# Kernel optimization log

Measured on AMD Instinct MI355X. Metric: run time of the kernel, lower is better.

The kernel has to match this reference:

```python
import jax, jax.numpy as jnp
import numpy as np

DIM = 1024
NUM_HEADS = 16
HEAD_DIM = DIM // NUM_HEADS
SCALE = HEAD_DIM ** (-0.5)


def alibi_slopes(num_heads):
    x = (2 ** 8) ** (1.0 / num_heads)
    return jnp.array([1.0 / x ** (i + 1) for i in range(num_heads)], dtype=jnp.float32)


def setup_inputs() -> dict:
    key = jax.random.key(0)
    ks = jax.random.split(key, 6)
    B, N = 2, 2048
    x = jax.random.normal(ks[0], (B, N, DIM), dtype=jnp.float32)
    s = DIM ** -0.5
    Wq = jax.random.normal(ks[1], (DIM, DIM), dtype=jnp.float32) * s
    Wk = jax.random.normal(ks[2], (DIM, DIM), dtype=jnp.float32) * s
    Wv = jax.random.normal(ks[3], (DIM, DIM), dtype=jnp.float32) * s
    Wp = jax.random.normal(ks[4], (DIM, DIM), dtype=jnp.float32) * s
    bp = jnp.zeros((DIM,), dtype=jnp.float32)
    return {"x": x, "Wq": Wq, "Wk": Wk, "Wv": Wv, "Wp": Wp, "bp": bp}


def reference(x, Wq, Wk, Wv, Wp, bp):
    B, N, C = x.shape
    H, D = NUM_HEADS, HEAD_DIM
    # Linear layers use torch convention: y = x @ W.T
    q = (x @ Wq.T).reshape(B, N, H, D).transpose(0, 2, 1, 3)  # [B,H,N,D]
    k = (x @ Wk.T).reshape(B, N, H, D).transpose(0, 2, 1, 3)
    v = (x @ Wv.T).reshape(B, N, H, D).transpose(0, 2, 1, 3)
    # ALiBi bias: slopes[h] * (j - i), shape [H,N,N]
    rel = (jnp.arange(N)[None, :] - jnp.arange(N)[:, None]).astype(jnp.float32)
    bias = alibi_slopes(H)[:, None, None] * rel  # [H,N,N]
    # NOTE: original code DIVIDES by scale (= head_dim**-0.5), i.e. multiplies by sqrt(D)
    score = jnp.einsum("bhnd,bhmd->bhnm", q, k) / SCALE + bias[None]
    attn = jax.nn.softmax(score, axis=-1)
    out = jnp.einsum("bhnm,bhmd->bhnd", attn, v)
    out = out.transpose(0, 2, 1, 3).reshape(B, N, C)
    return out @ Wp.T + bp
```

## Files before the change

### kernel.cpp

```cpp
#include <hip/hip_runtime.h>
#include <hip/hip_bf16.h>
#include <cstdint>
#include <cstddef>

#define BB 2
#define NN 2048
#define CC 1024
#define HH 16
#define DD 64
#define MM (BB*NN)

typedef __attribute__((ext_vector_type(8))) _Float16 half8;
typedef __attribute__((ext_vector_type(4))) _Float16 half4;
typedef __attribute__((ext_vector_type(4))) float f32x4;

__device__ __forceinline__ float exp2_fast(float x) {
    float r; asm("v_exp_f32 %0, %1" : "=v"(r) : "v"(x)); return r;
}

__device__ __forceinline__ void gl_lds16(const void* g, void* l) {
    __builtin_amdgcn_global_load_lds(
        (const __attribute__((address_space(1))) unsigned int*)g,
        (__attribute__((address_space(3))) unsigned int*)l, 16, 0, 0);
}

__global__ __launch_bounds__(256) void cvtAll(
    const float* __restrict__ x, const float* __restrict__ wq,
    const float* __restrict__ wk, const float* __restrict__ wv,
    const float* __restrict__ wp, _Float16* __restrict__ X16,
    _Float16* __restrict__ W16) {
    const int NX4 = MM * CC / 4;
    const int NW4 = CC * CC / 4;
    int i = blockIdx.x * 256 + threadIdx.x;
    const float4* src;
    half4* dst;
    if (i < NX4) {
        src = (const float4*)x + i;
        dst = (half4*)X16 + i;
    } else {
        int j = i - NX4;
        int s = j >> 18, off = j & (NW4 - 1);
        const float* wsel = (s == 0) ? wq : (s == 1) ? wk : (s == 2) ? wv : wp;
        src = (const float4*)wsel + off;
        dst = (half4*)(W16 + (size_t)s * CC * CC) + off;
    }
    float4 v = *src;
    half4 h = { (_Float16)v.x, (_Float16)v.y, (_Float16)v.z, (_Float16)v.w };
    *dst = h;
}

__global__ __launch_bounds__(256) void gemmQKV(
    const _Float16* __restrict__ A, const _Float16* __restrict__ B,
    _Float16* __restrict__ QH, _Float16* __restrict__ KH,
    _Float16* __restrict__ VT, float qscale) {
    __shared__ _Float16 sA[128 * 64];
    __shared__ _Float16 sB[128 * 64];
    const int K = CC;

    const int t = threadIdx.x;
    const int id = blockIdx.y * gridDim.x + blockIdx.x;
    const int xcd = id & 7, kk = id >> 3;
    const int bm = xcd * 4 + (kk & 3);
    const int bn = kk >> 2;
    const int w = t >> 6, lane = t & 63;
    const int wr = (w >> 1) * 64, wc = (w & 1) * 64;
    const int lr = lane & 15, lg = lane >> 4;

    f32x4 acc[4][4];
#pragma unroll
    for (int a = 0; a < 4; ++a)
#pragma unroll
        for (int b2 = 0; b2 < 4; ++b2)
#pragma unroll
            for (int e = 0; e < 4; ++e) acc[a][b2][e] = 0.f;

    for (int kt = 0; kt < K; kt += 64) {
#pragma unroll
        for (int p = 0; p < 4; ++p) {
            int u = p * 256 + t;
            int rowu = u >> 3, su = (u & 7) ^ (rowu & 7);
            gl_lds16(A + (size_t)(bm * 128 + rowu) * K + kt + su * 8, sA + u * 8);
            gl_lds16(B + (size_t)(bn * 128 + rowu) * K + kt + su * 8, sB + u * 8);
        }
        __syncthreads();

#pragma unroll
        for (int c = 0; c < 2; ++c) {
            half8 af[4], bf[4];
#pragma unroll
            for (int f = 0; f < 4; ++f) {
                int ra = wr + f * 16 + lr;
                af[f] = *(const half8*)((const char*)sA + ((ra * 128 + c * 64 + lg * 16) ^ ((ra & 7) << 4)));
                int rb = wc + f * 16 + lr;
                bf[f] = *(const half8*)((const char*)sB + ((rb * 128 + c * 64 + lg * 16) ^ ((rb & 7) << 4)));
            }
#pragma unroll
            for (int fi = 0; fi < 4; ++fi)
#pragma unroll
                for (int fj = 0; fj < 4; ++fj)
                    acc[fi][fj] = __builtin_amdgcn_mfma_f32_16x16x32_f16(af[fi], bf[fj], acc[fi][fj], 0, 0, 0);
        }
        __syncthreads();
    }

#pragma unroll
    for (int fi = 0; fi < 4; ++fi)
#pragma unroll
        for (int fj = 0; fj < 4; ++fj) {
            int col = bn * 128 + wc + fj * 16 + lr;
            int sel = col >> 10, c10 = col & 1023;
            int h2 = c10 >> 6, d2 = c10 & 63;
            int rowb = bm * 128 + wr + fi * 16 + lg * 4;
            int b2 = rowb >> 11, n2 = rowb & (NN - 1);
            if (sel == 0) {
#pragma unroll
                for (int e = 0; e < 4; ++e)
                    QH[((size_t)(b2 * HH + h2) * NN + n2 + e) * DD + d2] =
                        (_Float16)(acc[fi][fj][e] * qscale);
            } else if (sel == 1) {
#pragma unroll
                for (int e = 0; e < 4; ++e)
                    KH[((size_t)(b2 * HH + h2) * NN + n2 + e) * DD + d2] =
                        (_Float16)acc[fi][fj][e];
            } else {
                half4 pk = { (_Float16)acc[fi][fj][0], (_Float16)acc[fi][fj][1],
                             (_Float16)acc[fi][fj][2], (_Float16)acc[fi][fj][3] };
                *(half4*)(VT + ((size_t)(b2 * HH + h2) * DD + d2) * NN + n2) = pk;
            }
        }
}

__global__ __launch_bounds__(256) void gemmPROJ(
    const _Float16* __restrict__ A, const _Float16* __restrict__ B,
    const float* __restrict__ bias, float* __restrict__ Cout) {
    __shared__ _Float16 sA[128 * 64];
    __shared__ _Float16 sB[64 * 64];
    const int K = CC, N = CC;

    const int t = threadIdx.x;
    const int id = blockIdx.y * gridDim.x + blockIdx.x;
    const int xcd = id & 7, kk = id >> 3;
    const int bm = xcd * 4 + (kk & 3);
    const int bn = kk >> 2;
    const int w = t >> 6, lane = t & 63;
    const int wr = (w >> 1) * 64, wc = (w & 1) * 32;
    const int lr = lane & 15, lg = lane >> 4;

    f32x4 acc[4][2];
#pragma unroll
    for (int a = 0; a < 4; ++a)
#pragma unroll
        for (int b2 = 0; b2 < 2; ++b2)
#pragma unroll
            for (int e = 0; e < 4; ++e) acc[a][b2][e] = 0.f;

    for (int kt = 0; kt < K; kt += 64) {
#pragma unroll
        for (int p = 0; p < 4; ++p) {
            int u = p * 256 + t;
            int rowu = u >> 3, su = (u & 7) ^ (rowu & 7);
            gl_lds16(A + (size_t)(bm * 128 + rowu) * K + kt + su * 8, sA + u * 8);
        }
#pragma unroll
        for (int p = 0; p < 2; ++p) {
            int u = p * 256 + t;
            int rowu = u >> 3, su = (u & 7) ^ (rowu & 7);
            gl_lds16(B + (size_t)(bn * 64 + rowu) * K + kt + su * 8, sB + u * 8);
        }
        __syncthreads();

#pragma unroll
        for (int c = 0; c < 2; ++c) {
            half8 af[4], bf[2];
#pragma unroll
            for (int f = 0; f < 4; ++f) {
                int ra = wr + f * 16 + lr;
                af[f] = *(const half8*)((const char*)sA + ((ra * 128 + c * 64 + lg * 16) ^ ((ra & 7) << 4)));
            }
#pragma unroll
            for (int f = 0; f < 2; ++f) {
                int rb = wc + f * 16 + lr;
                bf[f] = *(const half8*)((const char*)sB + ((rb * 128 + c * 64 + lg * 16) ^ ((rb & 7) << 4)));
            }
#pragma unroll
            for (int fi = 0; fi < 4; ++fi)
#pragma unroll
                for (int fj = 0; fj < 2; ++fj)
                    acc[fi][fj] = __builtin_amdgcn_mfma_f32_16x16x32_f16(af[fi], bf[fj], acc[fi][fj], 0, 0, 0);
        }
        __syncthreads();
    }

#pragma unroll
    for (int fi = 0; fi < 4; ++fi)
#pragma unroll
        for (int fj = 0; fj < 2; ++fj)
#pragma unroll
            for (int e = 0; e < 4; ++e) {
                int row = bm * 128 + wr + fi * 16 + lg * 4 + e;
                int col = bn * 64 + wc + fj * 16 + lr;
                Cout[(size_t)row * N + col] = acc[fi][fj][e] + bias[col];
            }
}

__global__ __launch_bounds__(256, 8) void attn16(
    const _Float16* __restrict__ Qh, const _Float16* __restrict__ Kh,
    const _Float16* __restrict__ Vt, _Float16* __restrict__ AO) {
    __shared__ _Float16 sK[2][64 * 64];
    __shared__ _Float16 sV[2][64 * 64];
    __shared__ _Float16 sP[4][16 * 64];

    const int t = threadIdx.x, w = t >> 6, lane = t & 63;
    const int lr = lane & 15, lg = lane >> 4;
    const int bh = blockIdx.x, qb = blockIdx.y;
    const int b = bh >> 4, h = bh & 15;
    const int i0 = qb * 64;
    const size_t baseND = (size_t)bh * NN * DD;
    const size_t baseDN = (size_t)bh * DD * NN;

    half8 qf[2];
    {
        const size_t qoff = baseND + (size_t)(i0 + w * 16 + lr) * DD;
        qf[0] = *(const half8*)(Qh + qoff + 0 * 32 + lg * 8);
        qf[1] = *(const half8*)(Qh + qoff + 1 * 32 + lg * 8);
    }

    f32x4 accO[4];
#pragma unroll
    for (int e = 0; e < 4; ++e)
        accO[e][0] = accO[e][1] = accO[e][2] = accO[e][3] = 0.f;
    float m_run = -INFINITY, l_run = 0.f;

    const float slope2 = exp2f(-0.5f * (float)(h + 1)) * 1.44269504f;
    const float s64 = slope2 * 64.f;
    f32x4 cini[4];
#pragma unroll
    for (int ct = 0; ct < 4; ++ct)
#pragma unroll
        for (int e = 0; e < 4; ++e)
            cini[ct][e] = slope2 * (float)(ct * 16 + lg * 4 + e);

    auto stage = [&](int buf, int jt) {
#pragma unroll
        for (int p = 0; p < 2; ++p) {
            int u = p * 256 + t;
            int rowu = u >> 3, su = (u & 7) ^ (rowu & 7);
            gl_lds16(Kh + baseND + (size_t)(jt * 64 + rowu) * DD + su * 8, &sK[buf][u * 8]);
            gl_lds16(Vt + baseDN + (size_t)rowu * NN + jt * 64 + su * 8, &sV[buf][u * 8]);
        }
    };

    stage(0, 0);
    __syncthreads();
    int cur = 0;
    float tb = 0.f;

    for (int jt = 0; jt < NN / 64; ++jt) {
        if (jt + 1 < NN / 64) stage(cur ^ 1, jt + 1);

        f32x4 s[4];
#pragma unroll
        for (int ct = 0; ct < 4; ++ct)
#pragma unroll
            for (int e = 0; e < 4; ++e) s[ct][e] = tb + cini[ct][e];

        __builtin_amdgcn_s_setprio(1);
#pragma unroll
        for (int ct = 0; ct < 4; ++ct)
#pragma unroll
            for (int c = 0; c < 2; ++c) {
                int row = ct * 16 + lr;
                half8 kf = *(const half8*)((const char*)&sK[cur][0] +
                    ((row * 128 + c * 64 + lg * 16) ^ ((row & 7) << 4)));
                s[ct] = __builtin_amdgcn_mfma_f32_16x16x32_f16(kf, qf[c], s[ct], 0, 0, 0);
            }
        __builtin_amdgcn_s_setprio(0);

        float x0 = fmaxf(fmaxf(s[0][0], s[0][1]), fmaxf(s[0][2], s[0][3]));
        float x1 = fmaxf(fmaxf(s[1][0], s[1][1]), fmaxf(s[1][2], s[1][3]));
        float x2 = fmaxf(fmaxf(s[2][0], s[2][1]), fmaxf(s[2][2], s[2][3]));
        float x3 = fmaxf(fmaxf(s[3][0], s[3][1]), fmaxf(s[3][2], s[3][3]));
        float mx = fmaxf(fmaxf(x0, x1), fmaxf(x2, x3));
        mx = fmaxf(mx, __shfl_xor(mx, 16, 64));
        mx = fmaxf(mx, __shfl_xor(mx, 32, 64));
        float mnew = fmaxf(m_run, mx);
        float al = exp2_fast(m_run - mnew);
#pragma unroll
        for (int ct = 0; ct < 4; ++ct)
#pragma unroll
            for (int e = 0; e < 4; ++e) s[ct][e] = exp2_fast(s[ct][e] - mnew);
        float y0 = (s[0][0] + s[0][1]) + (s[0][2] + s[0][3]);
        float y1 = (s[1][0] + s[1][1]) + (s[1][2] + s[1][3]);
        float y2 = (s[2][0] + s[2][1]) + (s[2][2] + s[2][3]);
        float y3 = (s[3][0] + s[3][1]) + (s[3][2] + s[3][3]);
        float sum = (y0 + y1) + (y2 + y3);
        sum += __shfl_xor(sum, 16, 64);
        sum += __shfl_xor(sum, 32, 64);
        m_run = mnew;
        l_run = l_run * al + sum;

#pragma unroll
        for (int ct = 0; ct < 4; ++ct) {
            unsigned plo = __builtin_bit_cast(unsigned,
                __builtin_amdgcn_cvt_pkrtz(s[ct][0], s[ct][1]));
            unsigned phi = __builtin_bit_cast(unsigned,
                __builtin_amdgcn_cvt_pkrtz(s[ct][2], s[ct][3]));
            uint2 pk = { plo, phi };
            *(uint2*)((char*)sP[w] + ((lr * 128 + ct * 32 + lg * 8) ^ ((lr & 7) << 4))) = pk;
        }

#pragma unroll
        for (int ctd = 0; ctd < 4; ++ctd)
#pragma unroll
            for (int e = 0; e < 4; ++e) accO[ctd][e] *= al;

        half8 pb0 = *(const half8*)((const char*)sP[w] + ((lr * 128 + 0 * 64 + lg * 16) ^ ((lr & 7) << 4)));
        half8 pb1 = *(const half8*)((const char*)sP[w] + ((lr * 128 + 1 * 64 + lg * 16) ^ ((lr & 7) << 4)));
        __builtin_amdgcn_s_setprio(1);
#pragma unroll
        for (int ctd = 0; ctd < 4; ++ctd)
#pragma unroll
            for (int c = 0; c < 2; ++c) {
                int row = ctd * 16 + lr;
                half8 vf = *(const half8*)((const char*)&sV[cur][0] +
                    ((row * 128 + c * 64 + lg * 16) ^ ((row & 7) << 4)));
                accO[ctd] = __builtin_amdgcn_mfma_f32_16x16x32_f16(vf, c ? pb1 : pb0, accO[ctd], 0, 0, 0);
            }
        __builtin_amdgcn_s_setprio(0);

        __syncthreads();
        cur ^= 1;
        tb += s64;
    }

    float rl = 1.0f / l_run;
    const size_t obase = ((size_t)b * NN + i0 + w * 16 + lr) * CC + h * DD;
#pragma unroll
    for (int ctd = 0; ctd < 4; ++ctd) {
        half4 ov = { (_Float16)(accO[ctd][0] * rl), (_Float16)(accO[ctd][1] * rl),
                     (_Float16)(accO[ctd][2] * rl), (_Float16)(accO[ctd][3] * rl) };
        *(half4*)(AO + obase + ctd * 16 + lg * 4) = ov;
    }
}

extern "C" void kernel_launch(void* const* d_in, const int* in_sizes, int n_in,
                              void* d_out, int out_size, void* d_ws, size_t ws_size,
                              hipStream_t stream) {
    const float* x  = (const float*)d_in[0];
    const float* Wq = (const float*)d_in[1];
    const float* Wk = (const float*)d_in[2];
    const float* Wv = (const float*)d_in[3];
    const float* Wp = (const float*)d_in[4];
    const float* bp = (const float*)d_in[5];
    float* out = (float*)d_out;

    char* ws = (char*)d_ws;
    const size_t MB = 1024 * 1024;
    _Float16* X16 = (_Float16*)(ws + 0 * MB);
    _Float16* W16 = (_Float16*)(ws + 8 * MB);
    _Float16* QH  = (_Float16*)(ws + 16 * MB);
    _Float16* KH  = (_Float16*)(ws + 24 * MB);
    _Float16* VT  = (_Float16*)(ws + 32 * MB);
    _Float16* AO  = (_Float16*)(ws + 40 * MB);
    _Float16* WP16 = W16 + 3 * 1024 * 1024;

    cvtAll<<<8192, 256, 0, stream>>>(x, Wq, Wk, Wv, Wp, X16, W16);

    const float QSCALE = 8.0f * 1.44269504f;
    gemmQKV<<<dim3(3 * CC / 128, MM / 128), 256, 0, stream>>>(X16, W16, QH, KH, VT, QSCALE);

    attn16<<<dim3(BB * HH, NN / 64), 256, 0, stream>>>(QH, KH, VT, AO);

    gemmPROJ<<<dim3(CC / 64, MM / 128), 256, 0, stream>>>(AO, WP16, bp, out);
}
```

Before: 143.6 us.

## Split attention into producer and consumer warps with pipelined QK and PV

Rewrites the attention kernel as warp-specialized: four producer waves compute QK^T scores and the softmax for 32 query rows each, while four consumer waves do the PV MFMAs one tile behind. Probabilities and rescale factors pass through double-buffered LDS. Each block now covers 128 queries with 512 threads, which halves K/V reloads per query. The cost is more LDS, fewer blocks, and a possible imbalance between producer and consumer work.

```diff
diff --git a/kernel.cpp b/kernel.cpp
--- a/kernel.cpp
+++ b/kernel.cpp
@@ -203,143 +203,181 @@
             }
 }
 
-__global__ __launch_bounds__(256, 8) void attn16(
+__global__ __launch_bounds__(512, 4) void attnPC(
     const _Float16* __restrict__ Qh, const _Float16* __restrict__ Kh,
     const _Float16* __restrict__ Vt, _Float16* __restrict__ AO) {
     __shared__ _Float16 sK[2][64 * 64];
     __shared__ _Float16 sV[2][64 * 64];
-    __shared__ _Float16 sP[4][16 * 64];
+    __shared__ _Float16 sP[2][4][32 * 64];
+    __shared__ float sAl[2][4][32];
+    __shared__ float sL[4][32];
 
     const int t = threadIdx.x, w = t >> 6, lane = t & 63;
     const int lr = lane & 15, lg = lane >> 4;
     const int bh = blockIdx.x, qb = blockIdx.y;
     const int b = bh >> 4, h = bh & 15;
-    const int i0 = qb * 64;
+    const int i0 = qb * 128;
     const size_t baseND = (size_t)bh * NN * DD;
     const size_t baseDN = (size_t)bh * DD * NN;
-
-    half8 qf[2];
-    {
-        const size_t qoff = baseND + (size_t)(i0 + w * 16 + lr) * DD;
-        qf[0] = *(const half8*)(Qh + qoff + 0 * 32 + lg * 8);
-        qf[1] = *(const half8*)(Qh + qoff + 1 * 32 + lg * 8);
-    }
-
-    f32x4 accO[4];
-#pragma unroll
-    for (int e = 0; e < 4; ++e)
-        accO[e][0] = accO[e][1] = accO[e][2] = accO[e][3] = 0.f;
-    float m_run = -INFINITY, l_run = 0.f;
+    const bool isProd = (w < 4);
+    const int pw = w & 3;
 
     const float slope2 = exp2f(-0.5f * (float)(h + 1)) * 1.44269504f;
-    const float s64 = slope2 * 64.f;
-    f32x4 cini[4];
-#pragma unroll
-    for (int ct = 0; ct < 4; ++ct)
-#pragma unroll
-        for (int e = 0; e < 4; ++e)
-            cini[ct][e] = slope2 * (float)(ct * 16 + lg * 4 + e);
-
-    auto stage = [&](int buf, int jt) {
-#pragma unroll
-        for (int p = 0; p < 2; ++p) {
-            int u = p * 256 + t;
-            int rowu = u >> 3, su = (u & 7) ^ (rowu & 7);
-            gl_lds16(Kh + baseND + (size_t)(jt * 64 + rowu) * DD + su * 8, &sK[buf][u * 8]);
-            gl_lds16(Vt + baseDN + (size_t)rowu * NN + jt * 64 + su * 8, &sV[buf][u * 8]);
-        }
+    const float s64v = slope2 * 64.f;
+    const float s16v = slope2 * 16.f;
+    float cini0[4];
+#pragma unroll
+    for (int e = 0; e < 4; ++e) cini0[e] = slope2 * (float)(lg * 4 + e);
+
+    auto stageK = [&](int buf, int jt) {
+        int rowu = t >> 3, su = (t & 7) ^ (rowu & 7);
+        gl_lds16(Kh + baseND + (size_t)(jt * 64 + rowu) * DD + su * 8, &sK[buf][t * 8]);
     };
-
-    stage(0, 0);
-    __syncthreads();
-    int cur = 0;
-    float tb = 0.f;
-
-    for (int jt = 0; jt < NN / 64; ++jt) {
-        if (jt + 1 < NN / 64) stage(cur ^ 1, jt + 1);
-
-        f32x4 s[4];
-#pragma unroll
-        for (int ct = 0; ct < 4; ++ct)
-#pragma unroll
-            for (int e = 0; e < 4; ++e) s[ct][e] = tb + cini[ct][e];
-
+    auto stageV = [&](int buf, int jt) {
+        int rowu = t >> 3, su = (t & 7) ^ (rowu & 7);
+        gl_lds16(Vt + baseDN + (size_t)rowu * NN + jt * 64 + su * 8, &sV[buf][t * 8]);
+    };
+
+    half8 qf[2][2];
+    float m_run[2], l_run[2], tbp = 0.f;
+    f32x4 accO[2][4];
+
+    if (isProd) {
+#pragma unroll
+        for (int u = 0; u < 2; ++u) {
+            const size_t qoff = baseND + (size_t)(i0 + pw * 32 + u * 16 + lr) * DD;
+            qf[u][0] = *(const half8*)(Qh + qoff + 0 * 32 + lg * 8);
+            qf[u][1] = *(const half8*)(Qh + qoff + 1 * 32 + lg * 8);
+        }
+        m_run[0] = m_run[1] = -INFINITY;
+        l_run[0] = l_run[1] = 0.f;
+    } else {
+#pragma unroll
+        for (int u = 0; u < 2; ++u)
+#pragma unroll
+            for (int c2 = 0; c2 < 4; ++c2)
+                accO[u][c2][0] = accO[u][c2][1] = accO[u][c2][2] = accO[u][c2][3] = 0.f;
+    }
+
+    auto prodStep = [&](int pb, int kb) {
+        f32x4 s0[4], s1[4];
+#pragma unroll
+        for (int ct = 0; ct < 4; ++ct) {
+            float base = tbp + s16v * (float)ct;
+#pragma unroll
+            for (int e = 0; e < 4; ++e) { s0[ct][e] = base + cini0[e]; s1[ct][e] = s0[ct][e]; }
+        }
         __builtin_amdgcn_s_setprio(1);
 #pragma unroll
         for (int ct = 0; ct < 4; ++ct)
 #pragma unroll
             for (int c = 0; c < 2; ++c) {
                 int row = ct * 16 + lr;
-                half8 kf = *(const half8*)((const char*)&sK[cur][0] +
+                half8 kf = *(const half8*)((const char*)&sK[kb][0] +
                     ((row * 128 + c * 64 + lg * 16) ^ ((row & 7) << 4)));
-                s[ct] = __builtin_amdgcn_mfma_f32_16x16x32_f16(kf, qf[c], s[ct], 0, 0, 0);
+                s0[ct] = __builtin_amdgcn_mfma_f32_16x16x32_f16(kf, qf[0][c], s0[ct], 0, 0, 0);
+                s1[ct] = __builtin_amdgcn_mfma_f32_16x16x32_f16(kf, qf[1][c], s1[ct], 0, 0, 0);
             }
         __builtin_amdgcn_s_setprio(0);
-
-        float x0 = fmaxf(fmaxf(s[0][0], s[0][1]), fmaxf(s[0][2], s[0][3]));
-        float x1 = fmaxf(fmaxf(s[1][0], s[1][1]), fmaxf(s[1][2], s[1][3]));
-        float x2 = fmaxf(fmaxf(s[2][0], s[2][1]), fmaxf(s[2][2], s[2][3]));
-        float x3 = fmaxf(fmaxf(s[3][0], s[3][1]), fmaxf(s[3][2], s[3][3]));
-        float mx = fmaxf(fmaxf(x0, x1), fmaxf(x2, x3));
-        mx = fmaxf(mx, __shfl_xor(mx, 16, 64));
-        mx = fmaxf(mx, __shfl_xor(mx, 32, 64));
-        float mnew = fmaxf(m_run, mx);
-        float al = exp2_fast(m_run - mnew);
-#pragma unroll
-        for (int ct = 0; ct < 4; ++ct)
-#pragma unroll
-            for (int e = 0; e < 4; ++e) s[ct][e] = exp2_fast(s[ct][e] - mnew);
-        float y0 = (s[0][0] + s[0][1]) + (s[0][2] + s[0][3]);
-        float y1 = (s[1][0] + s[1][1]) + (s[1][2] + s[1][3]);
-        float y2 = (s[2][0] + s[2][1]) + (s[2][2] + s[2][3]);
-        float y3 = (s[3][0] + s[3][1]) + (s[3][2] + s[3][3]);
-        float sum = (y0 + y1) + (y2 + y3);
-        sum += __shfl_xor(sum, 16, 64);
-        sum += __shfl_xor(sum, 32, 64);
-        m_run = mnew;
-        l_run = l_run * al + sum;
-
-#pragma unroll
-        for (int ct = 0; ct < 4; ++ct) {
-            unsigned plo = __builtin_bit_cast(unsigned,
-                __builtin_amdgcn_cvt_pkrtz(s[ct][0], s[ct][1]));
-            unsigned phi = __builtin_bit_cast(unsigned,
-                __builtin_amdgcn_cvt_pkrtz(s[ct][2], s[ct][3]));
-            uint2 pk = { plo, phi };
-            *(uint2*)((char*)sP[w] + ((lr * 128 + ct * 32 + lg * 8) ^ ((lr & 7) << 4))) = pk;
-        }
-
-#pragma unroll
-        for (int ctd = 0; ctd < 4; ++ctd)
-#pragma unroll
-            for (int e = 0; e < 4; ++e) accO[ctd][e] *= al;
-
-        half8 pb0 = *(const half8*)((const char*)sP[w] + ((lr * 128 + 0 * 64 + lg * 16) ^ ((lr & 7) << 4)));
-        half8 pb1 = *(const half8*)((const char*)sP[w] + ((lr * 128 + 1 * 64 + lg * 16) ^ ((lr & 7) << 4)));
+#pragma unroll
+        for (int u = 0; u < 2; ++u) {
+            f32x4* s = u ? s1 : s0;
+            float x0 = fmaxf(fmaxf(s[0][0], s[0][1]), fmaxf(s[0][2], s[0][3]));
+            float x1 = fmaxf(fmaxf(s[1][0], s[1][1]), fmaxf(s[1][2], s[1][3]));
+            float x2 = fmaxf(fmaxf(s[2][0], s[2][1]), fmaxf(s[2][2], s[2][3]));
+            float x3 = fmaxf(fmaxf(s[3][0], s[3][1]), fmaxf(s[3][2], s[3][3]));
+            float mx = fmaxf(fmaxf(x0, x1), fmaxf(x2, x3));
+            mx = fmaxf(mx, __shfl_xor(mx, 16, 64));
+            mx = fmaxf(mx, __shfl_xor(mx, 32, 64));
+            float mnew = fmaxf(m_run[u], mx);
+            float al = exp2_fast(m_run[u] - mnew);
+#pragma unroll
+            for (int ct = 0; ct < 4; ++ct)
+#pragma unroll
+                for (int e = 0; e < 4; ++e) s[ct][e] = exp2_fast(s[ct][e] - mnew);
+            float y0 = (s[0][0] + s[0][1]) + (s[0][2] + s[0][3]);
+            float y1 = (s[1][0] + s[1][1]) + (s[1][2] + s[1][3]);
+            float y2 = (s[2][0] + s[2][1]) + (s[2][2] + s[2][3]);
+            float y3 = (s[3][0] + s[3][1]) + (s[3][2] + s[3][3]);
+            float sum = (y0 + y1) + (y2 + y3);
+            sum += __shfl_xor(sum, 16, 64);
+            sum += __shfl_xor(sum, 32, 64);
+            m_run[u] = mnew;
+            l_run[u] = l_run[u] * al + sum;
+            int row = u * 16 + lr;
+#pragma unroll
+            for (int ct = 0; ct < 4; ++ct) {
+                unsigned plo = __builtin_bit_cast(unsigned,
+                    __builtin_amdgcn_cvt_pkrtz(s[ct][0], s[ct][1]));
+                unsigned phi = __builtin_bit_cast(unsigned,
+                    __builtin_amdgcn_cvt_pkrtz(s[ct][2], s[ct][3]));
+                uint2 pk = { plo, phi };
+                *(uint2*)((char*)sP[pb][pw] + ((row * 128 + ct * 32 + lg * 8) ^ ((lr & 7) << 4))) = pk;
+            }
+            if (lg == 0) sAl[pb][pw][row] = al;
+        }
+        tbp += s64v;
+    };
+
+    auto consStep = [&](int vb) {
+        float al0 = sAl[vb][pw][lr];
+        float al1 = sAl[vb][pw][16 + lr];
+#pragma unroll
+        for (int c2 = 0; c2 < 4; ++c2)
+#pragma unroll
+            for (int e = 0; e < 4; ++e) { accO[0][c2][e] *= al0; accO[1][c2][e] *= al1; }
+        half8 pb0[2], pb1[2];
+#pragma unroll
+        for (int c = 0; c < 2; ++c) {
+            pb0[c] = *(const half8*)((const char*)sP[vb][pw] +
+                ((lr * 128 + c * 64 + lg * 16) ^ ((lr & 7) << 4)));
+            pb1[c] = *(const half8*)((const char*)sP[vb][pw] +
+                (((16 + lr) * 128 + c * 64 + lg * 16) ^ ((lr & 7) << 4)));
+        }
         __builtin_amdgcn_s_setprio(1);
 #pragma unroll
         for (int ctd = 0; ctd < 4; ++ctd)
 #pragma unroll
             for (int c = 0; c < 2; ++c) {
                 int row = ctd * 16 + lr;
-                half8 vf = *(const half8*)((const char*)&sV[cur][0] +
+                half8 vf = *(const half8*)((const char*)&sV[vb][0] +
                     ((row * 128 + c * 64 + lg * 16) ^ ((row & 7) << 4)));
-                accO[ctd] = __builtin_amdgcn_mfma_f32_16x16x32_f16(vf, c ? pb1 : pb0, accO[ctd], 0, 0, 0);
+                accO[0][ctd] = __builtin_amdgcn_mfma_f32_16x16x32_f16(vf, pb0[c], accO[0][ctd], 0, 0, 0);
+                accO[1][ctd] = __builtin_amdgcn_mfma_f32_16x16x32_f16(vf, pb1[c], accO[1][ctd], 0, 0, 0);
             }
         __builtin_amdgcn_s_setprio(0);
-
+    };
+
+    stageK(0, 0); stageK(1, 1); stageV(0, 0);
+    __syncthreads();
+    if (isProd) prodStep(0, 0);
+    __syncthreads();
+
+    for (int j = 0; j < 32; ++j) {
+        if (j + 2 < 32) stageK(j & 1, j + 2);
+        if (j + 1 < 32) stageV((j + 1) & 1, j + 1);
+        if (isProd) {
+            if (j + 1 < 32) prodStep((j + 1) & 1, (j + 1) & 1);
+        } else {
+            consStep(j & 1);
+        }
         __syncthreads();
-        cur ^= 1;
-        tb += s64;
-    }
-
-    float rl = 1.0f / l_run;
-    const size_t obase = ((size_t)b * NN + i0 + w * 16 + lr) * CC + h * DD;
-#pragma unroll
-    for (int ctd = 0; ctd < 4; ++ctd) {
-        half4 ov = { (_Float16)(accO[ctd][0] * rl), (_Float16)(accO[ctd][1] * rl),
-                     (_Float16)(accO[ctd][2] * rl), (_Float16)(accO[ctd][3] * rl) };
-        *(half4*)(AO + obase + ctd * 16 + lg * 4) = ov;
+    }
+
+    if (isProd && lg == 0) { sL[pw][lr] = l_run[0]; sL[pw][16 + lr] = l_run[1]; }
+    __syncthreads();
+    if (!isProd) {
+#pragma unroll
+        for (int u = 0; u < 2; ++u) {
+            float rl = 1.0f / sL[pw][u * 16 + lr];
+            const size_t obase = ((size_t)b * NN + i0 + pw * 32 + u * 16 + lr) * CC + h * DD;
+#pragma unroll
+            for (int ctd = 0; ctd < 4; ++ctd) {
+                half4 ov = { (_Float16)(accO[u][ctd][0] * rl), (_Float16)(accO[u][ctd][1] * rl),
+                             (_Float16)(accO[u][ctd][2] * rl), (_Float16)(accO[u][ctd][3] * rl) };
+                *(half4*)(AO + obase + ctd * 16 + lg * 4) = ov;
+            }
+        }
     }
 }
 
@@ -369,7 +407,7 @@
     const float QSCALE = 8.0f * 1.44269504f;
     gemmQKV<<<dim3(3 * CC / 128, MM / 128), 256, 0, stream>>>(X16, W16, QH, KH, VT, QSCALE);
 
-    attn16<<<dim3(BB * HH, NN / 64), 256, 0, stream>>>(QH, KH, VT, AO);
+    attnPC<<<dim3(BB * HH, NN / 128), 512, 0, stream>>>(QH, KH, VT, AO);
 
     gemmPROJ<<<dim3(CC / 64, MM / 128), 256, 0, stream>>>(AO, WP16, bp, out);
 }
```

After: 137.8 us (median of 4 runs). 1.04x faster.
